# Kernel tuning notes

Hardware: AMD Instinct MI355X
Metric: run time of the kernel (lower is better)

Reference implementation:

```python
import jax, jax.numpy as jnp
import numpy as np

N_NODES = 50000
N_EDGES = 200000
NODE_DIM = 160     # node feat dim (divisible by 5 per wrapper slicing)
EDGE_DIM = 64      # latent edge feat dim
RAW_EDGE_DIM = 8   # raw geometric edge attributes
HID = 256          # hidden dim of edge/node update MLPs
ENC_HID = 128      # hidden dim of EASP edge encoder
N_ITER = 3
ENC_IN = 2 * NODE_DIM + RAW_EDGE_DIM                 # 328
EDGE_IN = 2 * 2 * NODE_DIM + 2 * EDGE_DIM            # 768 (reattach -> factor 2)
MSG_IN = 2 * NODE_DIM + EDGE_DIM                     # 384 (reattach node + edge)


def _ln(x, g, b):
    mu = jnp.mean(x, axis=-1, keepdims=True)
    v = jnp.var(x, axis=-1, keepdims=True)
    return (x - mu) * jax.lax.rsqrt(v + 1e-5) * g + b


def setup_inputs() -> dict:
    key = jax.random.key(0)
    ks = jax.random.split(key, 24)

    def w(k, shape):
        return (jax.random.normal(k, shape, jnp.float32) / np.sqrt(shape[0])).astype(jnp.float32)

    return {
        'x': jax.random.normal(ks[0], (N_NODES, NODE_DIM), jnp.float32),
        'edge_attr': jax.random.normal(ks[1], (N_EDGES, RAW_EDGE_DIM), jnp.float32),
        # EASP edge encoder MLP
        'enc_W1': w(ks[2], (ENC_IN, ENC_HID)), 'enc_b1': jnp.zeros((ENC_HID,), jnp.float32),
        'enc_W2': w(ks[3], (ENC_HID, EDGE_DIM)), 'enc_b2': jnp.zeros((EDGE_DIM,), jnp.float32),
        # EdgeCNN edge update MLP
        'eW1': w(ks[4], (EDGE_IN, HID)), 'eb1': jnp.zeros((HID,), jnp.float32),
        'eW2': w(ks[5], (HID, EDGE_DIM)), 'eb2': jnp.zeros((EDGE_DIM,), jnp.float32),
        # AttentionNodeUpdateNet: per-edge message MLP + attention vector + node out
        'mW1': w(ks[6], (MSG_IN, HID)), 'mb1': jnp.zeros((HID,), jnp.float32),
        'att_v': w(ks[7], (HID,)),
        'nW1': w(ks[8], (HID, NODE_DIM)), 'nb1': jnp.zeros((NODE_DIM,), jnp.float32),
        # shared LayerNorms (ModuleList([layer]*n_iter) shares one layer)
        'ln_ng': jnp.ones((NODE_DIM,), jnp.float32), 'ln_nb': jnp.zeros((NODE_DIM,), jnp.float32),
        'ln_eg': jnp.ones((EDGE_DIM,), jnp.float32), 'ln_eb': jnp.zeros((EDGE_DIM,), jnp.float32),
        'edge_row': jax.random.randint(ks[9], (N_EDGES,), 0, N_NODES, jnp.int32),
        'edge_col': jax.random.randint(ks[10], (N_EDGES,), 0, N_NODES, jnp.int32),
    }


def reference(x, edge_attr, enc_W1, enc_b1, enc_W2, enc_b2, eW1, eb1, eW2, eb2,
              mW1, mb1, att_v, nW1, nb1, ln_ng, ln_nb, ln_eg, ln_eb,
              edge_row, edge_col):
    row, col = edge_row, edge_col
    # edge encoder: gather endpoints, encode raw edge attrs
    init_edge = jnp.concatenate([x[row], x[col], edge_attr], axis=1)  # [E, 328]
    init_edge = jnp.maximum(init_edge @ enc_W1 + enc_b1, 0.0) @ enc_W2 + enc_b2  # [E, 64]

    node_lat, edge_lat = x, init_edge
    for _ in range(N_ITER):
        nl = jnp.concatenate([x, node_lat], axis=1)            # reattach initial node feats [N, 320]
        el = jnp.concatenate([init_edge, edge_lat], axis=1)    # reattach initial edge feats [E, 128]
        # edge update: gather-concat-MLP
        e_in = jnp.concatenate([nl[row], nl[col], el], axis=1)  # [E, 768]
        new_edge = jnp.maximum(e_in @ eW1 + eb1, 0.0) @ eW2 + eb2  # [E, 64]
        # node update: per-edge message + segment-softmax attention + scatter agg
        msg = jnp.maximum(jnp.concatenate([nl[col], new_edge], axis=1) @ mW1 + mb1, 0.0)  # [E, 256]
        logit = jax.nn.leaky_relu(msg @ att_v, 0.2)             # [E]
        smax = jax.ops.segment_max(logit, row, num_segments=N_NODES)
        ex = jnp.exp(logit - smax[row])
        den = jax.ops.segment_sum(ex, row, num_segments=N_NODES)
        alpha = ex / (den[row] + 1e-16)
        agg = jax.ops.segment_sum(alpha[:, None] * msg, row, num_segments=N_NODES)  # [N, 256]
        new_node = agg @ nW1 + nb1                              # [N, 160]
        # residual skip + (shared) LayerNorm
        node_lat = _ln(x + new_node, ln_ng, ln_nb)
        edge_lat = _ln(init_edge + new_edge, ln_eg, ln_eb)
    return node_lat, edge_lat
```

## Files before the change

### kernel.cpp

```cpp
#include <hip/hip_runtime.h>
#include <stdint.h>

#define N_NODES 50000
#define N_EDGES 200000
#define SCAN_B 512

typedef __bf16 bf16_t;
typedef bf16_t bf16x8 __attribute__((ext_vector_type(8)));
typedef float f32x4 __attribute__((ext_vector_type(4)));

__device__ __forceinline__ float bf2f(ushort h) {
  union { unsigned int u; float f; } c; c.u = ((unsigned int)h) << 16; return c.f;
}
__device__ __forceinline__ ushort f2bf(float f) {
  union { float f; unsigned int u; } c; c.f = f;
  unsigned int r = (c.u >> 16) & 1u;
  c.u += 0x7fffu + r;
  return (ushort)(c.u >> 16);
}
__device__ __forceinline__ float wave_sum(float v) {
#pragma unroll
  for (int m = 32; m > 0; m >>= 1) v += __shfl_xor(v, m, 64);
  return v;
}

__global__ void detect_k(const ushort* x, unsigned int* flag) {
  int i = blockIdx.x * 256 + threadIdx.x;
  unsigned int cnt = 0;
  for (int j = i; j < 1000000; j += 64 * 256) {
    ushort v = x[j];
    if (((v & 0x7F80u) == 0x7F80u) && (v & 0x7Fu)) cnt++;
  }
  if (cnt) atomicAdd(flag, cnt);
}

__global__ void cvt_in_k(const void* src, ushort* dst, int n, const unsigned int* flag) {
  int i = blockIdx.x * 256 + threadIdx.x;
  if (i >= n) return;
  if (*flag >= 2) dst[i] = f2bf(((const float*)src)[i]);
  else            dst[i] = ((const ushort*)src)[i];
}

__global__ void transpose2_k(const void* W, ushort* Bt, int k0, int Ksrc, int Kpad,
                             int Wstride, const unsigned int* flag) {
  int k = blockIdx.x * 256 + threadIdx.x;
  int n = blockIdx.y;
  if (k >= Kpad) return;
  ushort v = 0;
  if (k < Ksrc) {
    if (*flag >= 2) v = f2bf(((const float*)W)[(size_t)(k0 + k) * Wstride + n]);
    else            v = ((const ushort*)W)[(size_t)(k0 + k) * Wstride + n];
  }
  Bt[(size_t)n * Kpad + k] = v;
}

__global__ void hist_k(const int* row, int* deg) {
  int e = blockIdx.x * 256 + threadIdx.x;
  if (e < N_EDGES) atomicAdd(&deg[row[e]], 1);
}
__global__ void scan_blk_k(const int* deg, int* off, int* bsum, int n) {
  __shared__ int s[SCAN_B];
  int i = blockIdx.x * SCAN_B + threadIdx.x;
  int v = (i < n) ? deg[i] : 0;
  s[threadIdx.x] = v;
  __syncthreads();
  for (int o = 1; o < SCAN_B; o <<= 1) {
    int t = (threadIdx.x >= o) ? s[threadIdx.x - o] : 0;
    __syncthreads();
    s[threadIdx.x] += t;
    __syncthreads();
  }
  if (i < n) off[i] = s[threadIdx.x] - v;
  if (threadIdx.x == SCAN_B - 1) bsum[blockIdx.x] = s[SCAN_B - 1];
}
__global__ void scan_top_k(int* bsum, int nb) {
  __shared__ int s[128];
  int v = (threadIdx.x < nb) ? bsum[threadIdx.x] : 0;
  s[threadIdx.x] = v;
  __syncthreads();
  for (int o = 1; o < 128; o <<= 1) {
    int t = (threadIdx.x >= o) ? s[threadIdx.x - o] : 0;
    __syncthreads();
    s[threadIdx.x] += t;
    __syncthreads();
  }
  if (threadIdx.x < nb) bsum[threadIdx.x] = s[threadIdx.x] - v;
}
__global__ void scan_add_k(int* off, const int* bsum, int n) {
  int i = blockIdx.x * 256 + threadIdx.x;
  if (i < n) off[i] += bsum[i >> 9];
  if (i == 0) off[n] = N_EDGES;
}
__global__ void fill_k(const int* row, const int* off, int* cur, int* perm) {
  int e = blockIdx.x * 256 + threadIdx.x;
  if (e >= N_EDGES) return;
  int r = row[e];
  int p = off[r] + atomicAdd(&cur[r], 1);
  perm[p] = e;
}

struct GemmP {
  const ushort* X;
  const ushort* L;
  const ushort* E2;
  const float*  Af;
  const int* row;
  const int* col;
  const ushort* Bt;
  const ushort* bias;
  const ushort* Cr;
  const ushort* Cc;
  long cst;
  ushort* outb;  long ob_stride;
  ushort* outb2; long ob2_stride;
  float*  outf;  long of_stride;
  long e2s;
  int M, K, Nw;
};

template <int MODE>
__device__ __forceinline__ uint4 load_a8(const GemmP& p, int e, int kg) {
  if (MODE == 0) {
    return *(const uint4*)(p.E2 + (size_t)e * p.e2s + kg);
  } else if (MODE == 5) {
    if (kg < 160) return *(const uint4*)(p.X + (size_t)e * 160 + kg);
    return *(const uint4*)(p.L + (size_t)e * 160 + (kg - 160));
  } else if (MODE == 7) {
    if (kg < 160) return *(const uint4*)(p.X + (size_t)e * 160 + kg);
    uint4 z; z.x = z.y = z.z = z.w = 0u; return z;
  } else if (MODE == 8) {
    if (kg < 8) return *(const uint4*)(p.E2 + (size_t)e * 8);
    uint4 z; z.x = z.y = z.z = z.w = 0u; return z;
  } else {
    const float* s = p.Af + (size_t)e * p.K + kg;
    f32x4 f0 = *(const f32x4*)s;
    f32x4 f1 = *(const f32x4*)(s + 4);
    union { ushort r[8]; uint4 u; } o;
    o.r[0] = f2bf(f0[0]); o.r[1] = f2bf(f0[1]); o.r[2] = f2bf(f0[2]); o.r[3] = f2bf(f0[3]);
    o.r[4] = f2bf(f1[0]); o.r[5] = f2bf(f1[1]); o.r[6] = f2bf(f1[2]); o.r[7] = f2bf(f1[3]);
    return o.u;
  }
}

template <int MODE, int CI, bool RELU, int NT>
__global__ __launch_bounds__(256) void gemm_k(GemmP p) {
  constexpr int BR = NT / 2;
  __shared__ __align__(16) ushort Asm[128 * 72];
  __shared__ __align__(16) ushort Bsm[NT * 16 * 72];
  const int t = threadIdx.x;
  const int w = t >> 6;
  const int l = t & 63;
  const int m0 = blockIdx.x * 128;
  const int n0 = blockIdx.y * (NT * 16);

  const int srow = t >> 1;
  const int sph = (t & 1) << 5;
  int e = m0 + srow;
  if (e >= p.M) e = p.M - 1;

  int bn_[BR], bk_[BR];
#pragma unroll
  for (int j = 0; j < BR; j++) {
    int cid = j * 256 + t;
    bn_[j] = cid >> 3;
    bk_[j] = (cid & 7) << 3;
  }

  const int mq = l & 15;
  const int qd = l >> 4;

  uint4 ar[4];
  uint4 br[BR];
  auto load_tile = [&](int k0) {
#pragma unroll
    for (int j = 0; j < 4; j++)
      ar[j] = load_a8<MODE>(p, e, k0 + sph + j * 8);
#pragma unroll
    for (int j = 0; j < BR; j++)
      br[j] = *(const uint4*)(p.Bt + (size_t)(n0 + bn_[j]) * p.K + k0 + bk_[j]);
  };

  load_tile(0);

  f32x4 acc[2][NT] = {};
  if (CI) {
#pragma unroll
    for (int mt = 0; mt < 2; mt++) {
#pragma unroll
      for (int i = 0; i < 4; i++) {
        int r = m0 + w * 32 + mt * 16 + qd * 4 + i;
        if (r >= p.M) r = p.M - 1;
        const ushort* pc = p.Cc + (size_t)p.col[r] * p.cst + n0 + mq;
        const ushort* pr = nullptr;
        if (CI == 1) pr = p.Cr + (size_t)p.row[r] * p.cst + n0 + mq;
#pragma unroll
        for (int nt = 0; nt < NT; nt++) {
          float v = bf2f(pc[nt * 16]);
          if (CI == 1) v += bf2f(pr[nt * 16]);
          acc[mt][nt][i] = v;
        }
      }
    }
  }

  const int kiters = p.K >> 6;
  for (int kt = 0; kt < kiters; kt++) {
    __syncthreads();
#pragma unroll
    for (int j = 0; j < 4; j++)
      *(uint4*)&Asm[srow * 72 + sph + j * 8] = ar[j];
#pragma unroll
    for (int j = 0; j < BR; j++)
      *(uint4*)&Bsm[bn_[j] * 72 + bk_[j]] = br[j];
    if (kt + 1 < kiters) load_tile((kt + 1) << 6);
    __syncthreads();
#pragma unroll
    for (int ph = 0; ph < 2; ph++) {
      uint4 ra0 = *(const uint4*)&Asm[(w * 32 + mq) * 72 + ph * 32 + qd * 8];
      uint4 ra1 = *(const uint4*)&Asm[(w * 32 + 16 + mq) * 72 + ph * 32 + qd * 8];
      bf16x8 af0 = __builtin_bit_cast(bf16x8, ra0);
      bf16x8 af1 = __builtin_bit_cast(bf16x8, ra1);
#pragma unroll
      for (int nt = 0; nt < NT; nt++) {
        uint4 rb = *(const uint4*)&Bsm[(nt * 16 + mq) * 72 + ph * 32 + qd * 8];
        bf16x8 bfv = __builtin_bit_cast(bf16x8, rb);
        acc[0][nt] = __builtin_amdgcn_mfma_f32_16x16x32_bf16(af0, bfv, acc[0][nt], 0, 0, 0);
        acc[1][nt] = __builtin_amdgcn_mfma_f32_16x16x32_bf16(af1, bfv, acc[1][nt], 0, 0, 0);
      }
    }
  }

#pragma unroll
  for (int mt = 0; mt < 2; mt++) {
#pragma unroll
    for (int nt = 0; nt < NT; nt++) {
      int c = n0 + nt * 16 + mq;
      float bv = bf2f(p.bias[c]);
#pragma unroll
      for (int i = 0; i < 4; i++) {
        int r = m0 + w * 32 + mt * 16 + qd * 4 + i;
        if (r >= p.M) continue;
        float v = acc[mt][nt][i] + bv;
        if (RELU) v = fmaxf(v, 0.0f);
        if (p.outb)  p.outb[(size_t)r * p.ob_stride + c] = f2bf(v);
        if (p.outb2) p.outb2[(size_t)r * p.ob2_stride + c] = f2bf(v);
        if (p.outf)  p.outf[(size_t)r * p.of_stride + c] = v;
      }
    }
  }
}

__global__ void copy_u4_k(const uint4* s, uint4* d, int n) {
  int i = blockIdx.x * 256 + threadIdx.x;
  if (i < n) d[i] = s[i];
}

__global__ void agg_csr_k(const ushort* msg, const ushort* att, const int* off,
                          const int* perm, float* agg) {
  int n = blockIdx.x * 4 + (threadIdx.x >> 6);
  int l = threadIdx.x & 63;
  if (n >= N_NODES) return;
  const int s0 = off[n], s1 = off[n + 1];
  ushort4 av = *(const ushort4*)(att + l * 4);
  const float a0 = bf2f(av.x), a1 = bf2f(av.y), a2 = bf2f(av.z), a3 = bf2f(av.w);
  float maxl = -1e30f;
  for (int j = s0; j < s1; j++) {
    int e = perm[j];
    ushort4 m = *(const ushort4*)(msg + (size_t)e * 256 + l * 4);
    float d = bf2f(m.x) * a0 + bf2f(m.y) * a1 + bf2f(m.z) * a2 + bf2f(m.w) * a3;
    d = wave_sum(d);
    float lg = (d > 0.0f) ? d : 0.2f * d;
    maxl = fmaxf(maxl, lg);
  }
  float den = 0.0f;
  f32x4 acc = {0.0f, 0.0f, 0.0f, 0.0f};
  for (int j = s0; j < s1; j++) {
    int e = perm[j];
    ushort4 m = *(const ushort4*)(msg + (size_t)e * 256 + l * 4);
    float m0 = bf2f(m.x), m1 = bf2f(m.y), m2 = bf2f(m.z), m3 = bf2f(m.w);
    float d = m0 * a0 + m1 * a1 + m2 * a2 + m3 * a3;
    d = wave_sum(d);
    float lg = (d > 0.0f) ? d : 0.2f * d;
    float ex = __expf(lg - maxl);
    den += ex;
    acc[0] += ex * m0; acc[1] += ex * m1; acc[2] += ex * m2; acc[3] += ex * m3;
  }
  float inv = 1.0f / (den + 1e-16f);
  f32x4 o = {acc[0] * inv, acc[1] * inv, acc[2] * inv, acc[3] * inv};
  *(f32x4*)(agg + (size_t)n * 256 + l * 4) = o;
}

__global__ void ln_node_k(const ushort* x, const float* nn, const ushort* g,
                          const ushort* b, ushort* nlat) {
  int n = blockIdx.x * 4 + (threadIdx.x >> 6);
  int l = threadIdx.x & 63;
  if (n >= N_NODES) return;
  size_t bx = (size_t)n * 160;
  float v0 = bf2f(x[bx + l]) + nn[bx + l];
  float v1 = bf2f(x[bx + 64 + l]) + nn[bx + 64 + l];
  float v2 = (l < 32) ? (bf2f(x[bx + 128 + l]) + nn[bx + 128 + l]) : 0.0f;
  float mu = wave_sum(v0 + v1 + v2) * (1.0f / 160.0f);
  float d0 = v0 - mu, d1 = v1 - mu;
  float d2 = (l < 32) ? (v2 - mu) : 0.0f;
  float var = wave_sum(d0 * d0 + d1 * d1 + d2 * d2) * (1.0f / 160.0f);
  float inv = rsqrtf(var + 1e-5f);
  nlat[bx + l]      = f2bf(d0 * inv * bf2f(g[l])      + bf2f(b[l]));
  nlat[bx + 64 + l] = f2bf(d1 * inv * bf2f(g[64 + l]) + bf2f(b[64 + l]));
  if (l < 32)
    nlat[bx + 128 + l] = f2bf(d2 * inv * bf2f(g[128 + l]) + bf2f(b[128 + l]));
}

__global__ void ln_edge_k(const ushort* g, const ushort* b, ushort* el) {
  int e = blockIdx.x * 4 + (threadIdx.x >> 6);
  int l = threadIdx.x & 63;
  if (e >= N_EDGES) return;
  float v = bf2f(el[(size_t)e * 128 + l]) + bf2f(el[(size_t)e * 128 + 64 + l]);
  float mu = wave_sum(v) * (1.0f / 64.0f);
  float d = v - mu;
  float var = wave_sum(d * d) * (1.0f / 64.0f);
  float inv = rsqrtf(var + 1e-5f);
  el[(size_t)e * 128 + 64 + l] = f2bf(d * inv * bf2f(g[l]) + bf2f(b[l]));
}

__global__ void out_node_k(const ushort* nlat, void* out, const unsigned int* flag) {
  int i = blockIdx.x * 256 + threadIdx.x;
  if (i >= N_NODES * 160) return;
  if (*flag >= 2) ((float*)out)[i] = bf2f(nlat[i]);
  else            ((ushort*)out)[i] = nlat[i];
}
__global__ void out_edge_k(const ushort* el, void* out, const unsigned int* flag) {
  int i = blockIdx.x * 256 + threadIdx.x;
  if (i >= N_EDGES * 64) return;
  int e = i >> 6, c = i & 63;
  ushort v = el[(size_t)e * 128 + 64 + c];
  size_t o = (size_t)N_NODES * 160 + i;
  if (*flag >= 2) ((float*)out)[o] = bf2f(v);
  else            ((ushort*)out)[o] = v;
}

extern "C" void kernel_launch(void* const* d_in, const int* in_sizes, int n_in,
                              void* d_out, int out_size, void* d_ws, size_t ws_size,
                              hipStream_t stream) {
  const void* x_r     = d_in[0];
  const void* eattr_r = d_in[1];
  const void* encW1   = d_in[2];
  const void* encb1_r = d_in[3];
  const void* encW2   = d_in[4];
  const void* encb2_r = d_in[5];
  const void* eW1     = d_in[6];
  const void* eb1_r   = d_in[7];
  const void* eW2     = d_in[8];
  const void* eb2_r   = d_in[9];
  const void* mW1     = d_in[10];
  const void* mb1_r   = d_in[11];
  const void* attv_r  = d_in[12];
  const void* nW1     = d_in[13];
  const void* nb1_r   = d_in[14];
  const void* lnng_r  = d_in[15];
  const void* lnnb_r  = d_in[16];
  const void* lneg_r  = d_in[17];
  const void* lneb_r  = d_in[18];
  const int* erow = (const int*)d_in[19];
  const int* ecol = (const int*)d_in[20];
  (void)in_sizes; (void)n_in;

  char* ws = (char*)d_ws;
  size_t off = 0;
  auto alloc = [&](size_t bytes) -> void* {
    void* p = ws + off;
    off = (off + bytes + 511) & ~(size_t)511;
    return p;
  };
  ushort* hm   = (ushort*)alloc((size_t)N_EDGES * 256 * 2);
  ushort* el   = (ushort*)alloc((size_t)N_EDGES * 128 * 2);
  float*  agg  = (float*)alloc((size_t)N_NODES * 256 * 4);
  ushort* xc   = (ushort*)alloc((size_t)N_NODES * 160 * 2);
  ushort* nlat = (ushort*)alloc((size_t)N_NODES * 160 * 2);
  ushort* Qc   = (ushort*)alloc((size_t)N_NODES * 256 * 2);
  int* degcur  = (int*)alloc((size_t)2 * N_NODES * 4);
  int* offcsr  = (int*)alloc((size_t)(N_NODES + 1) * 4);
  int* perm    = (int*)alloc((size_t)N_EDGES * 4);
  int* bsum    = (int*)alloc((size_t)128 * 4);
  ushort* BtPe = (ushort*)alloc((size_t)256 * 192 * 2);
  ushort* BtWenc = (ushort*)alloc((size_t)128 * 64 * 2);
  ushort* BtE2 = (ushort*)alloc((size_t)64 * 128 * 2);
  ushort* BtP  = (ushort*)alloc((size_t)512 * 320 * 2);
  ushort* BtWe = (ushort*)alloc((size_t)256 * 128 * 2);
  ushort* Bte2 = (ushort*)alloc((size_t)64 * 256 * 2);
  ushort* BtQ  = (ushort*)alloc((size_t)256 * 320 * 2);
  ushort* BtWm = (ushort*)alloc((size_t)256 * 64 * 2);
  ushort* Btn1 = (ushort*)alloc((size_t)160 * 256 * 2);
  ushort* pool = (ushort*)alloc((size_t)4096 * 2);
  unsigned int* flag = (unsigned int*)alloc(64);
  ushort* msg = hm;
  float*  nnf = (float*)hm;
  ushort* eac  = (ushort*)agg;
  ushort* Penc = (ushort*)((char*)agg + (size_t)N_EDGES * 8 * 2);
  ushort* Prc  = (ushort*)agg;
  ushort* zb   = pool + 2048;

  ushort* encb1c = pool;        ushort* encb2c = pool + 128;
  ushort* eb1c   = pool + 192;  ushort* eb2c   = pool + 448;
  ushort* mb1c   = pool + 512;  ushort* attvc  = pool + 768;
  ushort* nb1c   = pool + 1024; ushort* lnngc  = pool + 1184;
  ushort* lnnbc  = pool + 1344; ushort* lnegc  = pool + 1504;
  ushort* lnebc  = pool + 1568;

  if (off > ws_size) {
    hipMemsetAsync(d_out, 0, (size_t)out_size * 2, stream);
    return;
  }

  hipMemsetAsync(flag, 0, 64, stream);
  hipMemsetAsync(pool, 0, 4096 * 2, stream);
  hipMemsetAsync(degcur, 0, (size_t)2 * N_NODES * 4, stream);

  detect_k<<<64, 256, 0, stream>>>((const ushort*)x_r, flag);

  {
    int* deg = degcur;
    int* cur = degcur + N_NODES;
    const int nb = (N_NODES + SCAN_B - 1) / SCAN_B;
    hist_k<<<(N_EDGES + 255) / 256, 256, 0, stream>>>(erow, deg);
    scan_blk_k<<<nb, SCAN_B, 0, stream>>>(deg, offcsr, bsum, N_NODES);
    scan_top_k<<<1, 128, 0, stream>>>(bsum, nb);
    scan_add_k<<<(N_NODES + 255) / 256, 256, 0, stream>>>(offcsr, bsum, N_NODES);
    fill_k<<<(N_EDGES + 255) / 256, 256, 0, stream>>>(erow, offcsr, cur, perm);
  }

  cvt_in_k<<<(N_NODES * 160 + 255) / 256, 256, 0, stream>>>(x_r, xc, N_NODES * 160, flag);
  cvt_in_k<<<(N_EDGES * 8 + 255) / 256, 256, 0, stream>>>(eattr_r, eac, N_EDGES * 8, flag);
  cvt_in_k<<<1, 256, 0, stream>>>(encb1_r, encb1c, 128, flag);
  cvt_in_k<<<1, 256, 0, stream>>>(encb2_r, encb2c, 64, flag);
  cvt_in_k<<<1, 256, 0, stream>>>(eb1_r, eb1c, 256, flag);
  cvt_in_k<<<1, 256, 0, stream>>>(eb2_r, eb2c, 64, flag);
  cvt_in_k<<<1, 256, 0, stream>>>(mb1_r, mb1c, 256, flag);
  cvt_in_k<<<1, 256, 0, stream>>>(attv_r, attvc, 256, flag);
  cvt_in_k<<<1, 256, 0, stream>>>(nb1_r, nb1c, 160, flag);
  cvt_in_k<<<1, 256, 0, stream>>>(lnng_r, lnngc, 160, flag);
  cvt_in_k<<<1, 256, 0, stream>>>(lnnb_r, lnnbc, 160, flag);
  cvt_in_k<<<1, 256, 0, stream>>>(lneg_r, lnegc, 64, flag);
  cvt_in_k<<<1, 256, 0, stream>>>(lneb_r, lnebc, 64, flag);

  transpose2_k<<<dim3(1, 128), 256, 0, stream>>>(encW1, BtPe,             0, 160, 192, 128, flag);
  transpose2_k<<<dim3(1, 128), 256, 0, stream>>>(encW1, BtPe + 128 * 192, 160, 160, 192, 128, flag);
  transpose2_k<<<dim3(1, 128), 256, 0, stream>>>(encW1, BtWenc,           320, 8, 64, 128, flag);
  transpose2_k<<<dim3(1, 64), 256, 0, stream>>>(encW2, BtE2, 0, 128, 128, 64, flag);
  transpose2_k<<<dim3(2, 256), 256, 0, stream>>>(eW1, BtP,             0, 320, 320, 256, flag);
  transpose2_k<<<dim3(2, 256), 256, 0, stream>>>(eW1, BtP + 256 * 320, 320, 320, 320, 256, flag);
  transpose2_k<<<dim3(1, 256), 256, 0, stream>>>(eW1, BtWe, 640, 128, 128, 256, flag);
  transpose2_k<<<dim3(1, 64), 256, 0, stream>>>(eW2, Bte2, 0, 256, 256, 64, flag);
  transpose2_k<<<dim3(2, 256), 256, 0, stream>>>(mW1, BtQ, 0, 320, 320, 256, flag);
  transpose2_k<<<dim3(1, 256), 256, 0, stream>>>(mW1, BtWm, 320, 64, 64, 256, flag);
  transpose2_k<<<dim3(1, 160), 256, 0, stream>>>(nW1, Btn1, 0, 256, 256, 160, flag);

  copy_u4_k<<<(N_NODES * 160 / 8 + 255) / 256, 256, 0, stream>>>(
      (const uint4*)xc, (uint4*)nlat, N_NODES * 160 / 8);

  const int gE = (N_EDGES + 127) / 128;
  const int gN = (N_NODES + 127) / 128;

  {
    GemmP p{};
    p.X = xc; p.Bt = BtPe; p.bias = zb;
    p.outb = Penc; p.ob_stride = 256;
    p.M = N_NODES; p.K = 192; p.Nw = 256;
    gemm_k<7, 0, false, 8><<<dim3(gN, 2), 256, 0, stream>>>(p);
  }
  {
    GemmP p{};
    p.E2 = eac; p.row = erow; p.col = ecol;
    p.Cr = Penc; p.Cc = Penc + 128; p.cst = 256;
    p.Bt = BtWenc; p.bias = encb1c;
    p.outb = hm; p.ob_stride = 128;
    p.M = N_EDGES; p.K = 64; p.Nw = 128;
    gemm_k<8, 1, true, 8><<<dim3(gE, 1), 256, 0, stream>>>(p);
  }
  {
    GemmP p{};
    p.E2 = hm; p.e2s = 128; p.Bt = BtE2; p.bias = encb2c;
    p.outb = el; p.ob_stride = 128;
    p.outb2 = el + 64; p.ob2_stride = 128;
    p.M = N_EDGES; p.K = 128; p.Nw = 64;
    gemm_k<0, 0, false, 4><<<dim3(gE, 1), 256, 0, stream>>>(p);
  }

  for (int it = 0; it < 3; it++) {
    {
      GemmP p{};
      p.X = xc; p.L = nlat; p.Bt = BtP; p.bias = zb;
      p.outb = Prc; p.ob_stride = 512;
      p.M = N_NODES; p.K = 320; p.Nw = 512;
      gemm_k<5, 0, false, 8><<<dim3(gN, 4), 256, 0, stream>>>(p);
    }
    {
      GemmP p{};
      p.X = xc; p.L = nlat; p.Bt = BtQ; p.bias = zb;
      p.outb = Qc; p.ob_stride = 256;
      p.M = N_NODES; p.K = 320; p.Nw = 256;
      gemm_k<5, 0, false, 8><<<dim3(gN, 2), 256, 0, stream>>>(p);
    }
    {
      GemmP p{};
      p.E2 = el; p.e2s = 128; p.row = erow; p.col = ecol;
      p.Cr = Prc; p.Cc = Prc + 256; p.cst = 512;
      p.Bt = BtWe; p.bias = eb1c;
      p.outb = hm; p.ob_stride = 256;
      p.M = N_EDGES; p.K = 128; p.Nw = 256;
      gemm_k<0, 1, true, 8><<<dim3(gE, 2), 256, 0, stream>>>(p);
    }
    {
      GemmP p{};
      p.E2 = hm; p.e2s = 256; p.Bt = Bte2; p.bias = eb2c;
      p.outb = el + 64; p.ob_stride = 128;
      p.M = N_EDGES; p.K = 256; p.Nw = 64;
      gemm_k<0, 0, false, 4><<<dim3(gE, 1), 256, 0, stream>>>(p);
    }
    {
      GemmP p{};
      p.E2 = el + 64; p.e2s = 128; p.row = erow; p.col = ecol;
      p.Cc = Qc; p.cst = 256;
      p.Bt = BtWm; p.bias = mb1c;
      p.outb = msg; p.ob_stride = 256;
      p.M = N_EDGES; p.K = 64; p.Nw = 256;
      gemm_k<0, 2, true, 8><<<dim3(gE, 2), 256, 0, stream>>>(p);
    }
    ln_edge_k<<<N_EDGES / 4, 256, 0, stream>>>(lnegc, lnebc, el);
    agg_csr_k<<<(N_NODES + 3) / 4, 256, 0, stream>>>(msg, attvc, offcsr, perm, agg);
    {
      GemmP p{};
      p.Af = agg; p.Bt = Btn1; p.bias = nb1c;
      p.outf = nnf; p.of_stride = 160;
      p.M = N_NODES; p.K = 256; p.Nw = 160;
      gemm_k<4, 0, false, 10><<<dim3(gN, 1), 256, 0, stream>>>(p);
    }
    ln_node_k<<<(N_NODES + 3) / 4, 256, 0, stream>>>(xc, nnf, lnngc, lnnbc, nlat);
  }

  out_node_k<<<(N_NODES * 160 + 255) / 256, 256, 0, stream>>>(nlat, d_out, flag);
  out_edge_k<<<(N_EDGES * 64 + 255) / 256, 256, 0, stream>>>(el, d_out, flag);
  (void)out_size;
}
```

Baseline: 2.172 ms.

## Process edges in CSR-sorted order and stage GEMM epilogue through shared memory

All edge-level data (edge attributes, row/col indices, latent edge features, messages) is now kept in CSR order sorted by destination row. The aggregation kernel can then read messages contiguously instead of through perm, and the final edge output is scattered back through perm. Separately, the bf16 GEMM epilogue writes the tile into shared memory and then stores it with 16-byte coalesced writes instead of scattered 2-byte stores. This adds a gather kernel, extra index buffers and a larger shared-memory footprint per block.

```diff
diff --git a/kernel.cpp b/kernel.cpp
--- a/kernel.cpp
+++ b/kernel.cpp
@@ -39,6 +39,16 @@
   if (i >= n) return;
   if (*flag >= 2) dst[i] = f2bf(((const float*)src)[i]);
   else            dst[i] = ((const ushort*)src)[i];
+}
+
+__global__ void cvt_eattr_k(const void* src, const int* perm, ushort* dst,
+                            const unsigned int* flag) {
+  int i = blockIdx.x * 256 + threadIdx.x;
+  if (i >= N_EDGES * 8) return;
+  int e = i >> 3, j = i & 7;
+  size_t o = (size_t)perm[e] * 8 + j;
+  if (*flag >= 2) dst[i] = f2bf(((const float*)src)[o]);
+  else            dst[i] = ((const ushort*)src)[o];
 }
 
 __global__ void transpose2_k(const void* W, ushort* Bt, int k0, int Ksrc, int Kpad,
@@ -97,6 +107,14 @@
   int r = row[e];
   int p = off[r] + atomicAdd(&cur[r], 1);
   perm[p] = e;
+}
+__global__ void gather_rc_k(const int* row, const int* col, const int* perm,
+                            int* rs, int* cs) {
+  int e = blockIdx.x * 256 + threadIdx.x;
+  if (e >= N_EDGES) return;
+  int o = perm[e];
+  rs[e] = row[o];
+  cs[e] = col[o];
 }
 
 struct GemmP {
@@ -145,13 +163,15 @@
 template <int MODE, int CI, bool RELU, int NT>
 __global__ __launch_bounds__(256) void gemm_k(GemmP p) {
   constexpr int BR = NT / 2;
-  __shared__ __align__(16) ushort Asm[128 * 72];
-  __shared__ __align__(16) ushort Bsm[NT * 16 * 72];
+  constexpr int NTC = NT * 16;
+  __shared__ __align__(16) ushort smem[9216 + 1152 * NT];
+  ushort* Asm = smem;
+  ushort* Bsm = smem + 9216;
   const int t = threadIdx.x;
   const int w = t >> 6;
   const int l = t & 63;
   const int m0 = blockIdx.x * 128;
-  const int n0 = blockIdx.y * (NT * 16);
+  const int n0 = blockIdx.y * NTC;
 
   const int srow = t >> 1;
   const int sph = (t & 1) << 5;
@@ -230,23 +250,51 @@
     }
   }
 
-#pragma unroll
-  for (int mt = 0; mt < 2; mt++) {
-#pragma unroll
-    for (int nt = 0; nt < NT; nt++) {
-      int c = n0 + nt * 16 + mq;
-      float bv = bf2f(p.bias[c]);
-#pragma unroll
-      for (int i = 0; i < 4; i++) {
-        int r = m0 + w * 32 + mt * 16 + qd * 4 + i;
-        if (r >= p.M) continue;
-        float v = acc[mt][nt][i] + bv;
-        if (RELU) v = fmaxf(v, 0.0f);
-        if (p.outb)  p.outb[(size_t)r * p.ob_stride + c] = f2bf(v);
-        if (p.outb2) p.outb2[(size_t)r * p.ob2_stride + c] = f2bf(v);
-        if (p.outf)  p.outf[(size_t)r * p.of_stride + c] = v;
+  if (MODE == 4) {
+#pragma unroll
+    for (int mt = 0; mt < 2; mt++) {
+#pragma unroll
+      for (int nt = 0; nt < NT; nt++) {
+        int c = n0 + nt * 16 + mq;
+        float bv = bf2f(p.bias[c]);
+#pragma unroll
+        for (int i = 0; i < 4; i++) {
+          int r = m0 + w * 32 + mt * 16 + qd * 4 + i;
+          if (r >= p.M) continue;
+          float v = acc[mt][nt][i] + bv;
+          if (RELU) v = fmaxf(v, 0.0f);
+          p.outf[(size_t)r * p.of_stride + c] = v;
+        }
       }
     }
+  } else {
+    __syncthreads();
+    ushort* S = smem + w * (32 * NTC);
+#pragma unroll
+    for (int mt = 0; mt < 2; mt++) {
+#pragma unroll
+      for (int nt = 0; nt < NT; nt++) {
+        float bv = bf2f(p.bias[n0 + nt * 16 + mq]);
+#pragma unroll
+        for (int i = 0; i < 4; i++) {
+          float v = acc[mt][nt][i] + bv;
+          if (RELU) v = fmaxf(v, 0.0f);
+          S[(mt * 16 + qd * 4 + i) * NTC + nt * 16 + mq] = f2bf(v);
+        }
+      }
+    }
+    __syncthreads();
+#pragma unroll
+    for (int j = 0; j < NT; j++) {
+      int flat = (j * 64 + l) * 8;
+      int lr = flat / NTC, cc = flat % NTC;
+      int r = m0 + w * 32 + lr;
+      if (r < p.M) {
+        uint4 v = *(const uint4*)&S[lr * NTC + cc];
+        *(uint4*)(p.outb + (size_t)r * p.ob_stride + n0 + cc) = v;
+        if (p.outb2) *(uint4*)(p.outb2 + (size_t)r * p.ob2_stride + n0 + cc) = v;
+      }
+    }
   }
 }
 
@@ -256,7 +304,7 @@
 }
 
 __global__ void agg_csr_k(const ushort* msg, const ushort* att, const int* off,
-                          const int* perm, float* agg) {
+                          float* agg) {
   int n = blockIdx.x * 4 + (threadIdx.x >> 6);
   int l = threadIdx.x & 63;
   if (n >= N_NODES) return;
@@ -265,8 +313,7 @@
   const float a0 = bf2f(av.x), a1 = bf2f(av.y), a2 = bf2f(av.z), a3 = bf2f(av.w);
   float maxl = -1e30f;
   for (int j = s0; j < s1; j++) {
-    int e = perm[j];
-    ushort4 m = *(const ushort4*)(msg + (size_t)e * 256 + l * 4);
+    ushort4 m = *(const ushort4*)(msg + (size_t)j * 256 + l * 4);
     float d = bf2f(m.x) * a0 + bf2f(m.y) * a1 + bf2f(m.z) * a2 + bf2f(m.w) * a3;
     d = wave_sum(d);
     float lg = (d > 0.0f) ? d : 0.2f * d;
@@ -275,8 +322,7 @@
   float den = 0.0f;
   f32x4 acc = {0.0f, 0.0f, 0.0f, 0.0f};
   for (int j = s0; j < s1; j++) {
-    int e = perm[j];
-    ushort4 m = *(const ushort4*)(msg + (size_t)e * 256 + l * 4);
+    ushort4 m = *(const ushort4*)(msg + (size_t)j * 256 + l * 4);
     float m0 = bf2f(m.x), m1 = bf2f(m.y), m2 = bf2f(m.z), m3 = bf2f(m.w);
     float d = m0 * a0 + m1 * a1 + m2 * a2 + m3 * a3;
     d = wave_sum(d);
@@ -328,12 +374,13 @@
   if (*flag >= 2) ((float*)out)[i] = bf2f(nlat[i]);
   else            ((ushort*)out)[i] = nlat[i];
 }
-__global__ void out_edge_k(const ushort* el, void* out, const unsigned int* flag) {
+__global__ void out_edge_k(const ushort* el, const int* perm, void* out,
+                           const unsigned int* flag) {
   int i = blockIdx.x * 256 + threadIdx.x;
   if (i >= N_EDGES * 64) return;
   int e = i >> 6, c = i & 63;
   ushort v = el[(size_t)e * 128 + 64 + c];
-  size_t o = (size_t)N_NODES * 160 + i;
+  size_t o = (size_t)N_NODES * 160 + (size_t)perm[e] * 64 + c;
   if (*flag >= 2) ((float*)out)[o] = bf2f(v);
   else            ((ushort*)out)[o] = v;
 }
@@ -380,6 +427,8 @@
   int* degcur  = (int*)alloc((size_t)2 * N_NODES * 4);
   int* offcsr  = (int*)alloc((size_t)(N_NODES + 1) * 4);
   int* perm    = (int*)alloc((size_t)N_EDGES * 4);
+  int* rs      = (int*)alloc((size_t)N_EDGES * 4);
+  int* cs      = (int*)alloc((size_t)N_EDGES * 4);
   int* bsum    = (int*)alloc((size_t)128 * 4);
   ushort* BtPe = (ushort*)alloc((size_t)256 * 192 * 2);
   ushort* BtWenc = (ushort*)alloc((size_t)128 * 64 * 2);
@@ -426,10 +475,11 @@
     scan_top_k<<<1, 128, 0, stream>>>(bsum, nb);
     scan_add_k<<<(N_NODES + 255) / 256, 256, 0, stream>>>(offcsr, bsum, N_NODES);
     fill_k<<<(N_EDGES + 255) / 256, 256, 0, stream>>>(erow, offcsr, cur, perm);
+    gather_rc_k<<<(N_EDGES + 255) / 256, 256, 0, stream>>>(erow, ecol, perm, rs, cs);
   }
 
   cvt_in_k<<<(N_NODES * 160 + 255) / 256, 256, 0, stream>>>(x_r, xc, N_NODES * 160, flag);
-  cvt_in_k<<<(N_EDGES * 8 + 255) / 256, 256, 0, stream>>>(eattr_r, eac, N_EDGES * 8, flag);
+  cvt_eattr_k<<<(N_EDGES * 8 + 255) / 256, 256, 0, stream>>>(eattr_r, perm, eac, flag);
   cvt_in_k<<<1, 256, 0, stream>>>(encb1_r, encb1c, 128, flag);
   cvt_in_k<<<1, 256, 0, stream>>>(encb2_r, encb2c, 64, flag);
   cvt_in_k<<<1, 256, 0, stream>>>(eb1_r, eb1c, 256, flag);
@@ -469,7 +519,7 @@
   }
   {
     GemmP p{};
-    p.E2 = eac; p.row = erow; p.col = ecol;
+    p.E2 = eac; p.row = rs; p.col = cs;
     p.Cr = Penc; p.Cc = Penc + 128; p.cst = 256;
     p.Bt = BtWenc; p.bias = encb1c;
     p.outb = hm; p.ob_stride = 128;
@@ -502,7 +552,7 @@
     }
     {
       GemmP p{};
-      p.E2 = el; p.e2s = 128; p.row = erow; p.col = ecol;
+      p.E2 = el; p.e2s = 128; p.row = rs; p.col = cs;
       p.Cr = Prc; p.Cc = Prc + 256; p.cst = 512;
       p.Bt = BtWe; p.bias = eb1c;
       p.outb = hm; p.ob_stride = 256;
@@ -518,7 +568,7 @@
     }
     {
       GemmP p{};
-      p.E2 = el + 64; p.e2s = 128; p.row = erow; p.col = ecol;
+      p.E2 = el + 64; p.e2s = 128; p.row = rs; p.col = cs;
       p.Cc = Qc; p.cst = 256;
       p.Bt = BtWm; p.bias = mb1c;
       p.outb = msg; p.ob_stride = 256;
@@ -526,7 +576,7 @@
       gemm_k<0, 2, true, 8><<<dim3(gE, 2), 256, 0, stream>>>(p);
     }
     ln_edge_k<<<N_EDGES / 4, 256, 0, stream>>>(lnegc, lnebc, el);
-    agg_csr_k<<<(N_NODES + 3) / 4, 256, 0, stream>>>(msg, attvc, offcsr, perm, agg);
+    agg_csr_k<<<(N_NODES + 3) / 4, 256, 0, stream>>>(msg, attvc, offcsr, agg);
     {
       GemmP p{};
       p.Af = agg; p.Bt = Btn1; p.bias = nb1c;
@@ -538,6 +588,6 @@
   }
 
   out_node_k<<<(N_NODES * 160 + 255) / 256, 256, 0, stream>>>(nlat, d_out, flag);
-  out_edge_k<<<(N_EDGES * 64 + 255) / 256, 256, 0, stream>>>(el, d_out, flag);
+  out_edge_k<<<(N_EDGES * 64 + 255) / 256, 256, 0, stream>>>(el, perm, d_out, flag);
   (void)out_size;
 }
```

After: 1.814 ms. -16.5%, faster.
